# Kernel tuning notes

Hardware: AMD Instinct MI355X
Metric: run time of the kernel (lower is better)

## Reference

```python
import jax, jax.numpy as jnp
import numpy as np

CH = 256
C8 = CH // 8


def setup_inputs() -> dict:
    key = jax.random.key(0)
    ks = jax.random.split(key, 8)
    scale = 1.0 / np.sqrt(CH)
    x = jax.random.normal(ks[0], (8, CH, 64, 64), dtype=jnp.float32)
    Wq = jax.random.normal(ks[1], (C8, CH), dtype=jnp.float32) * scale
    bq = jnp.zeros((C8,), dtype=jnp.float32)
    Wk = jax.random.normal(ks[2], (C8, CH), dtype=jnp.float32) * scale
    bk = jnp.zeros((C8,), dtype=jnp.float32)
    Wv = jax.random.normal(ks[3], (CH, CH), dtype=jnp.float32) * scale
    bv = jnp.zeros((CH,), dtype=jnp.float32)
    gamma = jnp.full((1,), 0.1, dtype=jnp.float32)  # nonzero so output depends on attention path
    return {"x": x, "Wq": Wq, "bq": bq, "Wk": Wk, "bk": bk, "Wv": Wv, "bv": bv, "gamma": gamma}


def reference(x, Wq, bq, Wk, bk, Wv, bv, gamma):
    b, c, h, w = x.shape
    hw = h * w
    xf = x.reshape(b, c, hw)  # flatten spatial; 1x1 conv == channel matmul
    q = jnp.einsum('oc,bcn->bno', Wq, xf) + bq          # (b, hw, c/8)
    k = jnp.einsum('oc,bcn->bon', Wk, xf) + bk[None, :, None]  # (b, c/8, hw)
    v = jnp.einsum('oc,bcn->bon', Wv, xf) + bv[None, :, None]  # (b, c, hw)
    attn = jax.nn.softmax(jnp.einsum('bno,bom->bnm', q, k), axis=-1)  # (b, hw, hw)
    out = jnp.einsum('bcm,bnm->bcn', v, attn).reshape(b, c, h, w)
    return x + gamma * out
```

## Files before the change

### kernel.cpp

```cpp
#include <hip/hip_runtime.h>
#include <stdint.h>

constexpr int CHN = 256;
constexpr int HW  = 4096;

constexpr int VROW   = 72;
constexpr int VTILE  = 256 * VROW;
constexpr int HTILE  = 128 * VROW;
constexpr int VBATCH = 64 * VTILE;

typedef float f32x4   __attribute__((ext_vector_type(4)));
typedef float f32x16  __attribute__((ext_vector_type(16)));
typedef short bf16x8  __attribute__((ext_vector_type(8)));
typedef short s16x4   __attribute__((ext_vector_type(4)));

static __device__ __forceinline__ short f2bf(float f) {
  uint32_t u = __builtin_bit_cast(uint32_t, f);
  u += 0x7FFFu + ((u >> 16) & 1u);
  return (short)(u >> 16);
}

static __device__ __forceinline__ uint8_t f2fp8(float f) {
  return (uint8_t)__builtin_amdgcn_cvt_pk_fp8_f32(f, f, 0, false);
}

static __device__ __forceinline__ void gl16(const void* g, void* l) {
  __builtin_amdgcn_global_load_lds(
      (const __attribute__((address_space(1))) uint32_t*)g,
      (__attribute__((address_space(3))) uint32_t*)l, 16, 0, 0);
}

__global__ __launch_bounds__(256) void prep_kernel(
    const float* __restrict__ Wq, const float* __restrict__ Wk, const float* __restrict__ Wv,
    const float* __restrict__ bq, const float* __restrict__ bk, const float* __restrict__ bv,
    short* __restrict__ Wb, float* __restrict__ bcat) {
  int idx = blockIdx.x * 256 + threadIdx.x;
  if (idx < 320 * 256) {
    int r = idx >> 8, c = idx & 255;
    float w = (r < 256) ? Wv[idx]
            : (r < 288) ? Wq[(r - 256) * 256 + c]
                        : Wk[(r - 288) * 256 + c];
    Wb[idx] = f2bf(w);
  }
  if (idx < 320)
    bcat[idx] = (idx < 256) ? bv[idx] : (idx < 288) ? bq[idx - 256] : bk[idx - 288];
}

__global__ __launch_bounds__(320) void proj_kernel(
    const float* __restrict__ x, const short* __restrict__ Wb, const float* __restrict__ bcat,
    short* __restrict__ qw, short* __restrict__ kw, uint8_t* __restrict__ v8) {
  const int t    = threadIdx.x;
  const int b    = blockIdx.y;
  const int n0   = blockIdx.x * 64;
  const int lane = t & 63;
  const int w    = t >> 6;
  const int ln   = lane & 15;
  const int gp   = lane >> 4;

  const float* xb  = x + (size_t)b * CHN * HW + n0;
  const short* wbp = Wb + (w * 64 + ln) * 256 + gp * 8;

  const f32x4 zv = {0.f, 0.f, 0.f, 0.f};
  f32x4 acc[4][4];
#pragma unroll
  for (int i = 0; i < 4; ++i)
#pragma unroll
    for (int j = 0; j < 4; ++j) acc[i][j] = zv;

#pragma unroll 2
  for (int ks = 0; ks < 8; ++ks) {
    const int k0 = ks * 32;
    bf16x8 a[4];
#pragma unroll
    for (int i = 0; i < 4; ++i)
      a[i] = *(const bf16x8*)(wbp + i * 16 * 256 + k0);
    bf16x8 bxv[4];
#pragma unroll
    for (int j = 0; j < 4; ++j) {
      const float* xc = xb + (size_t)(k0 + gp * 8) * HW + 16 * j + ln;
#pragma unroll
      for (int e = 0; e < 8; ++e) bxv[j][e] = f2bf(xc[(size_t)e * HW]);
    }
#pragma unroll
    for (int i = 0; i < 4; ++i)
#pragma unroll
      for (int j = 0; j < 4; ++j)
        acc[i][j] = __builtin_amdgcn_mfma_f32_16x16x32_bf16(a[i], bxv[j], acc[i][j], 0, 0, 0);
  }

  if (w < 4) {
    uint8_t* vblob = v8 + ((size_t)(b * 64 + blockIdx.x)) * VTILE;
    const int phi = 8 * ((ln >> 2) & 1) + 4 * (ln >> 3) + (ln & 3);
#pragma unroll
    for (int i = 0; i < 4; ++i) {
#pragma unroll
      for (int r = 0; r < 4; ++r) {
        const int c = w * 64 + 16 * i + 4 * gp + r;
        const float bias = bcat[c];
#pragma unroll
        for (int j = 0; j < 4; ++j)
          vblob[c * VROW + 16 * j + phi] = f2fp8(acc[i][j][r] + bias);
      }
    }
  } else {
    constexpr float LOG2E = 1.44269504088896340736f;
#pragma unroll
    for (int j = 0; j < 4; ++j) {
      const size_t nrow = ((size_t)b * HW + n0 + 16 * j + ln) * 32;
#pragma unroll
      for (int i = 0; i < 2; ++i) {
        s16x4 pq, pk;
#pragma unroll
        for (int r = 0; r < 4; ++r) {
          pq[r] = f2bf((acc[i][j][r] + bcat[256 + 16 * i + 4 * gp + r]) * LOG2E);
          pk[r] = f2bf(acc[i + 2][j][r] + bcat[288 + 16 * i + 4 * gp + r]);
        }
        *(s16x4*)(qw + nrow + 16 * i + 4 * gp) = pq;
        *(s16x4*)(kw + nrow + 16 * i + 4 * gp) = pk;
      }
    }
  }
}

__global__ __launch_bounds__(256, 2) void attn_kernel(
    const float* __restrict__ x, const float* __restrict__ gamma,
    const short* __restrict__ qw, const short* __restrict__ kw,
    const uint8_t* __restrict__ v8, float* __restrict__ out) {
  __shared__ alignas(16) char sm[2 * HTILE];

  const int tid  = threadIdx.x;
  const int lane = tid & 63;
  const int wv   = tid >> 6;
  const int l5   = lane & 31;
  const int h    = lane >> 5;
  const int b    = blockIdx.x & 7;
  const int g    = (blockIdx.x >> 3) & 1;
  const int qt   = blockIdx.x >> 4;
  const int qbase = qt * 128;

  const short*   qb    = qw + (size_t)b * HW * 32;
  const short*   kb    = kw + (size_t)b * HW * 32;
  const uint8_t* vblob = v8 + (size_t)b * VBATCH + (size_t)g * HTILE;

  const short* qrow = qb + (size_t)(qbase + wv * 32 + l5) * 32 + h * 8;
  const bf16x8 qf0 = *(const bf16x8*)(qrow);
  const bf16x8 qf1 = *(const bf16x8*)(qrow + 16);

  f32x16 z16;
#pragma unroll
  for (int r = 0; r < 16; ++r) z16[r] = 0.f;
  f32x16 O[4];
#pragma unroll
  for (int ct = 0; ct < 4; ++ct) O[ct] = z16;
  float mrun = -1e30f, lrun = 0.f;

  auto stage = [&](int tile, char* lbuf) {
    const uint8_t* gt = vblob + (size_t)tile * VTILE;
#pragma unroll
    for (int j = 0; j < 3; ++j) {
      const int cidx = wv + 4 * j;
      if (cidx < 9)
        gl16(gt + cidx * 1024 + lane * 16, lbuf + cidx * 1024);
    }
  };

  stage(0, sm);
  asm volatile("" ::: "memory");
  const short* kfb = kb + (size_t)l5 * 32 + h * 8;
  bf16x8 kf00 = *(const bf16x8*)(kfb);
  bf16x8 kf01 = *(const bf16x8*)(kfb + 16);
  bf16x8 kf10 = *(const bf16x8*)(kfb + 1024);
  bf16x8 kf11 = *(const bf16x8*)(kfb + 1024 + 16);

  for (int it = 0; it < 64; ++it) {
    asm volatile("s_waitcnt vmcnt(4)" ::: "memory");
    __builtin_amdgcn_s_barrier();
    asm volatile("" ::: "memory");

    const char* buf = sm + (it & 1) * HTILE;
    if (it < 63) stage(it + 1, sm + ((it + 1) & 1) * HTILE);
    asm volatile("" ::: "memory");

    f32x16 s0 = __builtin_amdgcn_mfma_f32_32x32x16_bf16(kf00, qf0, z16, 0, 0, 0);
    s0 = __builtin_amdgcn_mfma_f32_32x32x16_bf16(kf01, qf1, s0, 0, 0, 0);
    f32x16 s1 = __builtin_amdgcn_mfma_f32_32x32x16_bf16(kf10, qf0, z16, 0, 0, 0);
    s1 = __builtin_amdgcn_mfma_f32_32x32x16_bf16(kf11, qf1, s1, 0, 0, 0);

    if (it < 63) {
      const short* kn = kfb + (size_t)(it + 1) * 2048;
      kf00 = *(const bf16x8*)(kn);
      kf01 = *(const bf16x8*)(kn + 16);
      kf10 = *(const bf16x8*)(kn + 1024);
      kf11 = *(const bf16x8*)(kn + 1024 + 16);
    }

    float tm[8];
#pragma unroll
    for (int r = 0; r < 8; ++r)
      tm[r] = fmaxf(fmaxf(s0[r], s0[r + 8]), fmaxf(s1[r], s1[r + 8]));
#pragma unroll
    for (int r = 0; r < 4; ++r) tm[r] = fmaxf(tm[r], tm[r + 4]);
    float tmax = fmaxf(fmaxf(tm[0], tm[2]), fmaxf(tm[1], tm[3]));
    tmax = fmaxf(tmax, __shfl_xor(tmax, 32));
    if (__any(tmax > mrun + 8.f)) {
      const float mnew = fmaxf(mrun, tmax);
      const float al = __builtin_amdgcn_exp2f(mrun - mnew);
      lrun *= al;
      mrun = mnew;
#pragma unroll
      for (int r = 0; r < 16; ++r) {
        const float ar = __shfl(al, (r & 3) + 8 * (r >> 2) + 4 * h);
#pragma unroll
        for (int ct = 0; ct < 4; ++ct) O[ct][r] *= ar;
      }
    }
#pragma unroll
    for (int r = 0; r < 16; ++r) {
      s0[r] = __builtin_amdgcn_exp2f(s0[r] - mrun);
      s1[r] = __builtin_amdgcn_exp2f(s1[r] - mrun);
    }
    float pp[8];
#pragma unroll
    for (int r = 0; r < 8; ++r)
      pp[r] = (s0[r] + s0[r + 8]) + (s1[r] + s1[r + 8]);
#pragma unroll
    for (int r = 0; r < 4; ++r) pp[r] += pp[r + 4];
    float ps = (pp[0] + pp[2]) + (pp[1] + pp[3]);
    ps += __shfl_xor(ps, 32);
    lrun += ps;

    const char* vbl = buf + l5 * VROW;
#pragma unroll
    for (int mt = 0; mt < 4; ++mt) {
      const int r0 = (mt & 1) * 8;
      int lo, hi;
      if (mt < 2) {
        lo = __builtin_amdgcn_cvt_pk_fp8_f32(s0[r0 + 0], s0[r0 + 1], 0,  false);
        lo = __builtin_amdgcn_cvt_pk_fp8_f32(s0[r0 + 2], s0[r0 + 3], lo, true);
        hi = __builtin_amdgcn_cvt_pk_fp8_f32(s0[r0 + 4], s0[r0 + 5], 0,  false);
        hi = __builtin_amdgcn_cvt_pk_fp8_f32(s0[r0 + 6], s0[r0 + 7], hi, true);
      } else {
        lo = __builtin_amdgcn_cvt_pk_fp8_f32(s1[r0 + 0], s1[r0 + 1], 0,  false);
        lo = __builtin_amdgcn_cvt_pk_fp8_f32(s1[r0 + 2], s1[r0 + 3], lo, true);
        hi = __builtin_amdgcn_cvt_pk_fp8_f32(s1[r0 + 4], s1[r0 + 5], 0,  false);
        hi = __builtin_amdgcn_cvt_pk_fp8_f32(s1[r0 + 6], s1[r0 + 7], hi, true);
      }
      const long long pa = (long long)(((uint64_t)(uint32_t)hi << 32) | (uint32_t)lo);
      const int vo = 16 * mt + 8 * h;
#pragma unroll
      for (int ct = 0; ct < 4; ++ct) {
        const long long vf = *(const long long*)(vbl + ct * (32 * VROW) + vo);
        O[ct] = __builtin_amdgcn_mfma_f32_32x32x16_fp8_fp8(pa, vf, O[ct], 0, 0, 0);
      }
    }
  }

  const float g0 = gamma[0];
  float linv[16];
#pragma unroll
  for (int r = 0; r < 16; ++r)
    linv[r] = g0 / __shfl(lrun, (r & 3) + 8 * (r >> 2) + 4 * h);

  float* eo = (float*)sm;
  for (int ct = 0; ct < 4; ++ct) {
    __syncthreads();
#pragma unroll
    for (int r = 0; r < 16; ++r)
      eo[l5 * 132 + wv * 32 + ((r & 3) + 8 * (r >> 2) + 4 * h)] = O[ct][r] * linv[r];
    __syncthreads();
    const int cl = tid >> 3, seg = tid & 7;
    const size_t gi = ((size_t)b * CHN + g * 128 + ct * 32 + cl) * HW + qbase + seg * 16;
#pragma unroll
    for (int u = 0; u < 4; ++u) {
      const f32x4 xv = *(const f32x4*)(x + gi + u * 4);
      const f32x4 ov = *(const f32x4*)(&eo[cl * 132 + seg * 16 + u * 4]);
      *(f32x4*)(out + gi + u * 4) = xv + ov;
    }
  }
}

extern "C" void kernel_launch(void* const* d_in, const int* in_sizes, int n_in,
                              void* d_out, int out_size, void* d_ws, size_t ws_size,
                              hipStream_t stream) {
  const float* x     = (const float*)d_in[0];
  const float* Wq    = (const float*)d_in[1];
  const float* bq    = (const float*)d_in[2];
  const float* Wk    = (const float*)d_in[3];
  const float* bk    = (const float*)d_in[4];
  const float* Wv    = (const float*)d_in[5];
  const float* bv    = (const float*)d_in[6];
  const float* gamma = (const float*)d_in[7];
  float* out = (float*)d_out;

  char* ws = (char*)d_ws;
  short*   qw   = (short*)(ws);
  short*   kw   = (short*)(ws + (2u << 20));
  uint8_t* v8   = (uint8_t*)(ws + (4u << 20));
  short*   Wb   = (short*)(ws + (20u << 20));
  float*   bcat = (float*)(ws + (20u << 20) + (256u << 10));

  prep_kernel<<<320, 256, 0, stream>>>(Wq, Wk, Wv, bq, bk, bv, Wb, bcat);
  proj_kernel<<<dim3(64, 8), 320, 0, stream>>>(x, Wb, bcat, qw, kw, v8);
  attn_kernel<<<512, 256, 0, stream>>>(x, gamma, qw, kw, v8, out);
}
```

Measured before the change: 132.9 us.

## Split attention over key range into two partials and merge with rescale

Splits the 64 key tiles into two halves, so the attention kernel launches 1024 blocks instead of 512. Each block writes bf16 partial outputs plus per-query max and sum, then a weight kernel and a merge kernel combine the halves and add the residual. The launch bound is raised to 4 blocks per SM. This targets low occupancy and the tail effect on a machine with many compute units, at the cost of extra global traffic for the partials (32MB of bf16 writes plus reads), two extra launches, and bf16 rounding of the partial outputs. The new path runs only when the workspace is at least 49MB, otherwise the old path is used.

```diff
diff --git a/kernel.cpp b/kernel.cpp
--- a/kernel.cpp
+++ b/kernel.cpp
@@ -19,11 +19,13 @@
   u += 0x7FFFu + ((u >> 16) & 1u);
   return (short)(u >> 16);
 }
-
+static __device__ __forceinline__ float bf2f(short s) {
+  uint32_t u = ((uint32_t)(uint16_t)s) << 16;
+  return __builtin_bit_cast(float, u);
+}
 static __device__ __forceinline__ uint8_t f2fp8(float f) {
   return (uint8_t)__builtin_amdgcn_cvt_pk_fp8_f32(f, f, 0, false);
 }
-
 static __device__ __forceinline__ void gl16(const void* g, void* l) {
   __builtin_amdgcn_global_load_lds(
       (const __attribute__((address_space(1))) uint32_t*)g,
@@ -122,10 +124,12 @@
   }
 }
 
-__global__ __launch_bounds__(256, 2) void attn_kernel(
+template <bool PART>
+__global__ __launch_bounds__(256, 4) void attn_kernel(
     const float* __restrict__ x, const float* __restrict__ gamma,
     const short* __restrict__ qw, const short* __restrict__ kw,
-    const uint8_t* __restrict__ v8, float* __restrict__ out) {
+    const uint8_t* __restrict__ v8, float* __restrict__ out,
+    short* __restrict__ pO, float* __restrict__ ml) {
   __shared__ alignas(16) char sm[2 * HTILE];
 
   const int tid  = threadIdx.x;
@@ -135,8 +139,11 @@
   const int h    = lane >> 5;
   const int b    = blockIdx.x & 7;
   const int g    = (blockIdx.x >> 3) & 1;
-  const int qt   = blockIdx.x >> 4;
+  const int s    = PART ? ((blockIdx.x >> 4) & 1) : 0;
+  const int qt   = PART ? (blockIdx.x >> 5) : (blockIdx.x >> 4);
   const int qbase = qt * 128;
+  const int S0    = s * 32;
+  constexpr int NT = PART ? 32 : 64;
 
   const short*   qb    = qw + (size_t)b * HW * 32;
   const short*   kb    = kw + (size_t)b * HW * 32;
@@ -164,21 +171,22 @@
     }
   };
 
-  stage(0, sm);
+  stage(S0, sm);
   asm volatile("" ::: "memory");
   const short* kfb = kb + (size_t)l5 * 32 + h * 8;
-  bf16x8 kf00 = *(const bf16x8*)(kfb);
-  bf16x8 kf01 = *(const bf16x8*)(kfb + 16);
-  bf16x8 kf10 = *(const bf16x8*)(kfb + 1024);
-  bf16x8 kf11 = *(const bf16x8*)(kfb + 1024 + 16);
-
-  for (int it = 0; it < 64; ++it) {
+  const short* k0p = kfb + (size_t)S0 * 2048;
+  bf16x8 kf00 = *(const bf16x8*)(k0p);
+  bf16x8 kf01 = *(const bf16x8*)(k0p + 16);
+  bf16x8 kf10 = *(const bf16x8*)(k0p + 1024);
+  bf16x8 kf11 = *(const bf16x8*)(k0p + 1024 + 16);
+
+  for (int it = 0; it < NT; ++it) {
     asm volatile("s_waitcnt vmcnt(4)" ::: "memory");
     __builtin_amdgcn_s_barrier();
     asm volatile("" ::: "memory");
 
     const char* buf = sm + (it & 1) * HTILE;
-    if (it < 63) stage(it + 1, sm + ((it + 1) & 1) * HTILE);
+    if (it < NT - 1) stage(S0 + it + 1, sm + ((it + 1) & 1) * HTILE);
     asm volatile("" ::: "memory");
 
     f32x16 s0 = __builtin_amdgcn_mfma_f32_32x32x16_bf16(kf00, qf0, z16, 0, 0, 0);
@@ -186,8 +194,8 @@
     f32x16 s1 = __builtin_amdgcn_mfma_f32_32x32x16_bf16(kf10, qf0, z16, 0, 0, 0);
     s1 = __builtin_amdgcn_mfma_f32_32x32x16_bf16(kf11, qf1, s1, 0, 0, 0);
 
-    if (it < 63) {
-      const short* kn = kfb + (size_t)(it + 1) * 2048;
+    if (it < NT - 1) {
+      const short* kn = kfb + (size_t)(S0 + it + 1) * 2048;
       kf00 = *(const bf16x8*)(kn);
       kf01 = *(const bf16x8*)(kn + 16);
       kf10 = *(const bf16x8*)(kn + 1024);
@@ -255,11 +263,17 @@
     }
   }
 
-  const float g0 = gamma[0];
+  if (PART && g == 0 && h == 0) {
+    const int q = qbase + wv * 32 + l5;
+    float* mp = ml + ((size_t)(s * 8 + b) * HW + q) * 2;
+    mp[0] = mrun;
+    mp[1] = lrun;
+  }
+  const float gsc = PART ? 1.0f : gamma[0];
   float linv[16];
 #pragma unroll
   for (int r = 0; r < 16; ++r)
-    linv[r] = g0 / __shfl(lrun, (r & 3) + 8 * (r >> 2) + 4 * h);
+    linv[r] = gsc / __shfl(lrun, (r & 3) + 8 * (r >> 2) + 4 * h);
 
   float* eo = (float*)sm;
   for (int ct = 0; ct < 4; ++ct) {
@@ -269,13 +283,67 @@
       eo[l5 * 132 + wv * 32 + ((r & 3) + 8 * (r >> 2) + 4 * h)] = O[ct][r] * linv[r];
     __syncthreads();
     const int cl = tid >> 3, seg = tid & 7;
-    const size_t gi = ((size_t)b * CHN + g * 128 + ct * 32 + cl) * HW + qbase + seg * 16;
-#pragma unroll
-    for (int u = 0; u < 4; ++u) {
-      const f32x4 xv = *(const f32x4*)(x + gi + u * 4);
-      const f32x4 ov = *(const f32x4*)(&eo[cl * 132 + seg * 16 + u * 4]);
-      *(f32x4*)(out + gi + u * 4) = xv + ov;
-    }
+    const int ch = g * 128 + ct * 32 + cl;
+    if (PART) {
+      short* pp8 = pO + (((size_t)(s * 8 + b) * CHN + ch) << 12) + qbase + seg * 16;
+#pragma unroll
+      for (int u = 0; u < 4; ++u) {
+        const f32x4 ov = *(const f32x4*)(&eo[cl * 132 + seg * 16 + u * 4]);
+        s16x4 pv;
+#pragma unroll
+        for (int e = 0; e < 4; ++e) pv[e] = f2bf(ov[e]);
+        *(s16x4*)(pp8 + u * 4) = pv;
+      }
+    } else {
+      const size_t gi = ((size_t)b * CHN + ch) * HW + qbase + seg * 16;
+#pragma unroll
+      for (int u = 0; u < 4; ++u) {
+        const f32x4 xv = *(const f32x4*)(x + gi + u * 4);
+        const f32x4 ov = *(const f32x4*)(&eo[cl * 132 + seg * 16 + u * 4]);
+        *(f32x4*)(out + gi + u * 4) = xv + ov;
+      }
+    }
+  }
+}
+
+__global__ __launch_bounds__(256) void wgt_kernel(
+    const float* __restrict__ ml, const float* __restrict__ gamma,
+    float* __restrict__ aw) {
+  const int i = blockIdx.x * 256 + threadIdx.x;
+  if (i >= 8 * HW) return;
+  const float m0 = ml[(size_t)i * 2], l0 = ml[(size_t)i * 2 + 1];
+  const float m1 = ml[(size_t)(8 * HW + i) * 2], l1 = ml[(size_t)(8 * HW + i) * 2 + 1];
+  const float mj = fmaxf(m0, m1);
+  const float w0 = l0 * __builtin_amdgcn_exp2f(m0 - mj);
+  const float w1 = l1 * __builtin_amdgcn_exp2f(m1 - mj);
+  const float gi = gamma[0] / (w0 + w1);
+  aw[(size_t)i * 2]     = w0 * gi;
+  aw[(size_t)i * 2 + 1] = w1 * gi;
+}
+
+__global__ __launch_bounds__(256) void merge_kernel(
+    const float* __restrict__ x, const short* __restrict__ pO,
+    const float* __restrict__ aw, float* __restrict__ out) {
+  const size_t base = ((size_t)blockIdx.x * 256 + threadIdx.x) * 16;
+  const int b  = (int)(base >> 20);
+  const int q0 = (int)(base & 4095);
+  const short* p0 = pO + ((base >> 12) << 12) + q0;
+  const short* p1 = p0 + ((size_t)8 * CHN << 12);
+  const float* ap = aw + ((size_t)b * HW + q0) * 2;
+  const float* xp = x + base;
+  float* op = out + base;
+#pragma unroll
+  for (int u = 0; u < 4; ++u) {
+    const f32x4 xv = *(const f32x4*)(xp + u * 4);
+    const s16x4 v0 = *(const s16x4*)(p0 + u * 4);
+    const s16x4 v1 = *(const s16x4*)(p1 + u * 4);
+    f32x4 ov;
+#pragma unroll
+    for (int e = 0; e < 4; ++e) {
+      const int qi = u * 4 + e;
+      ov[e] = xv[e] + ap[2 * qi] * bf2f(v0[e]) + ap[2 * qi + 1] * bf2f(v1[e]);
+    }
+    *(f32x4*)(op + u * 4) = ov;
   }
 }
 
@@ -296,10 +364,21 @@
   short*   qw   = (short*)(ws);
   short*   kw   = (short*)(ws + (2u << 20));
   uint8_t* v8   = (uint8_t*)(ws + (4u << 20));
-  short*   Wb   = (short*)(ws + (20u << 20));
-  float*   bcat = (float*)(ws + (20u << 20) + (256u << 10));
+  short*   Wb   = (short*)(ws + (14u << 20));
+  float*   bcat = (float*)(ws + (14u << 20) + (256u << 10));
+  short*   pO   = (short*)(ws + (15u << 20));
+  float*   ml   = (float*)(ws + (47u << 20));
+  float*   aw   = (float*)(ws + (48u << 20));
+
+  const bool part = (ws_size >= ((size_t)49 << 20));
 
   prep_kernel<<<320, 256, 0, stream>>>(Wq, Wk, Wv, bq, bk, bv, Wb, bcat);
   proj_kernel<<<dim3(64, 8), 320, 0, stream>>>(x, Wb, bcat, qw, kw, v8);
-  attn_kernel<<<512, 256, 0, stream>>>(x, gamma, qw, kw, v8, out);
-}
+  if (part) {
+    attn_kernel<true><<<1024, 256, 0, stream>>>(x, gamma, qw, kw, v8, out, pO, ml);
+    wgt_kernel<<<128, 256, 0, stream>>>(ml, gamma, aw);
+    merge_kernel<<<2048, 256, 0, stream>>>(x, pO, aw, out);
+  } else {
+    attn_kernel<false><<<512, 256, 0, stream>>>(x, gamma, qw, kw, v8, out, pO, ml);
+  }
+}
```

Result: slower. 221.9 us (+67.0%).
